# Kernel tuning notes

Measured on AMD Instinct MI355X. Metric: run time of the kernel, lower is better.

The kernel has to match this reference:

```python
import jax, jax.numpy as jnp
import numpy as np

B, S, H = 1, 2048, 4096
NQ, NKV, D = 32, 8, 128
N_REP = NQ // NKV
SCALE = 1.0 / np.sqrt(D)
SOFTCAP = 30.0
EPS = 1e-5


def _rotate_half(x):
    x1, x2 = jnp.split(x, 2, axis=-1)
    return jnp.concatenate([-x2, x1], axis=-1)


def _rms_norm(x, w, eps=EPS):
    xf = x.astype(jnp.float32)
    norm = xf * jax.lax.rsqrt(jnp.mean(xf * xf, axis=-1, keepdims=True) + eps)
    return (w * norm).astype(x.dtype)


def setup_inputs() -> dict:
    key = jax.random.key(0)
    ks = jax.random.split(key, 8)
    hidden_states = jax.random.normal(ks[0], (B, S, H), dtype=jnp.float32)
    # causal additive mask
    causal = jnp.tril(jnp.ones((S, S), dtype=bool))
    attention_mask = jnp.where(causal, 0.0, -1e9)[None, None].astype(jnp.float32)
    # RoPE cache
    inv_freq = 1.0 / (10000.0 ** (np.arange(0, D, 2, dtype=np.float32) / D))
    t = np.arange(S, dtype=np.float32)
    freqs = np.outer(t, inv_freq)                      # (S, D/2)
    emb = np.concatenate([freqs, freqs], axis=-1)      # (S, D)
    cos = jnp.asarray(np.cos(emb))[None, None]         # (1,1,S,D)
    sin = jnp.asarray(np.sin(emb))[None, None]
    # params
    std = 0.02
    wq = jax.random.normal(ks[1], (NQ * D, H), dtype=jnp.float32) * std
    wk = jax.random.normal(ks[2], (NKV * D, H), dtype=jnp.float32) * std
    wv = jax.random.normal(ks[3], (NKV * D, H), dtype=jnp.float32) * std
    wo = jax.random.normal(ks[4], (H, NQ * D), dtype=jnp.float32) * std
    pre_norm_w = jnp.ones((H,), dtype=jnp.float32)
    q_norm_w = jnp.ones((D,), dtype=jnp.float32)
    k_norm_w = jnp.ones((D,), dtype=jnp.float32)
    return {
        "hidden_states": hidden_states, "attention_mask": attention_mask,
        "cos": cos, "sin": sin, "pre_norm_w": pre_norm_w,
        "wq": wq, "wk": wk, "wv": wv, "wo": wo,
        "q_norm_w": q_norm_w, "k_norm_w": k_norm_w,
    }


def reference(hidden_states, attention_mask, cos, sin, pre_norm_w,
              wq, wk, wv, wo, q_norm_w, k_norm_w):
    residual = hidden_states
    h = _rms_norm(hidden_states, pre_norm_w)
    bsz, seq_len, _ = h.shape
    # projections -> (b, heads, s, d)
    q = jnp.einsum('bsh,eh->bse', h, wq).reshape(bsz, seq_len, NQ, D).transpose(0, 2, 1, 3)
    k = jnp.einsum('bsh,eh->bse', h, wk).reshape(bsz, seq_len, NKV, D).transpose(0, 2, 1, 3)
    v = jnp.einsum('bsh,eh->bse', h, wv).reshape(bsz, seq_len, NKV, D).transpose(0, 2, 1, 3)
    # QK RMSNorm over head_dim
    q = _rms_norm(q, q_norm_w)
    k = _rms_norm(k, k_norm_w)
    # RoPE (full head_dim)
    q = q * cos + _rotate_half(q) * sin
    k = k * cos + _rotate_half(k) * sin
    # GQA: repeat kv heads
    k_exp = jnp.repeat(k, N_REP, axis=1)  # (b, NQ, s, d)
    v_exp = jnp.repeat(v, N_REP, axis=1)
    scores = jnp.einsum('bhqd,bhkd->bhqk', q, k_exp) * SCALE
    scores = SOFTCAP * jnp.tanh(scores / SOFTCAP)
    scores = scores + attention_mask
    probs = jax.nn.softmax(scores.astype(jnp.float32), axis=-1).astype(q.dtype)
    attn = jnp.einsum('bhqk,bhkd->bhqd', probs, v_exp)
    attn = attn.transpose(0, 2, 1, 3).reshape(bsz, seq_len, NQ * D)
    out = jnp.einsum('bse,he->bsh', attn, wo)
    return residual + out
```

## Files before the change

### kernel.cpp

```cpp
#include <hip/hip_runtime.h>
#include <cstdint>

typedef __bf16 bf16;
typedef __bf16 bf16x8 __attribute__((ext_vector_type(8)));
typedef __bf16 bf16x4 __attribute__((ext_vector_type(4)));
typedef float  f32x4  __attribute__((ext_vector_type(4)));

#define SEQ  2048
#define HID  4096
#define DH   128
#define NQH  32
#define NKVH 8
#define RSCALE 0.08838834764831845f
#define SOFTCAP 30.0f
#define L2E 1.4426950408889634f

__device__ __forceinline__ void gl2lds16(const void* g, void* l) {
  __builtin_amdgcn_global_load_lds(
      (const __attribute__((address_space(1))) unsigned int*)g,
      (__attribute__((address_space(3))) unsigned int*)l, 16, 0, 0);
}

__global__ void cvt_kernel(const float* __restrict__ in, bf16* __restrict__ out, int n4) {
  const int stride = gridDim.x * blockDim.x;
  for (int i = blockIdx.x * blockDim.x + threadIdx.x; i < n4; i += stride) {
    const float4 v = ((const float4*)in)[i];
    bf16x4 o = { (bf16)v.x, (bf16)v.y, (bf16)v.z, (bf16)v.w };
    *(bf16x4*)(out + (size_t)i * 4) = o;
  }
}

__global__ void rmsnorm_kernel(const float* __restrict__ x, const float* __restrict__ w,
                               bf16* __restrict__ out) {
  const int s = blockIdx.x;
  const float* xr = x + (size_t)s * HID;
  float4 v[4];
  float ss = 0.f;
#pragma unroll
  for (int j = 0; j < 4; ++j) {
    v[j] = ((const float4*)xr)[threadIdx.x + j * 256];
    ss += v[j].x * v[j].x + v[j].y * v[j].y + v[j].z * v[j].z + v[j].w * v[j].w;
  }
#pragma unroll
  for (int m = 1; m < 64; m <<= 1) ss += __shfl_xor(ss, m);
  __shared__ float red[4];
  if ((threadIdx.x & 63) == 0) red[threadIdx.x >> 6] = ss;
  __syncthreads();
  const float rn = rsqrtf((red[0] + red[1] + red[2] + red[3]) * (1.f / HID) + 1e-5f);
  bf16* orow = out + (size_t)s * HID;
#pragma unroll
  for (int j = 0; j < 4; ++j) {
    const int idx = (threadIdx.x + j * 256) * 4;
    const float4 wv = ((const float4*)w)[threadIdx.x + j * 256];
    bf16x4 o = { (bf16)(v[j].x * rn * wv.x), (bf16)(v[j].y * rn * wv.y),
                 (bf16)(v[j].z * rn * wv.z), (bf16)(v[j].w * rn * wv.w) };
    *(bf16x4*)(orow + idx) = o;
  }
}

template<bool FINAL>
__global__ __launch_bounds__(256, 3)
void gemm_bt(const bf16* __restrict__ A, const bf16* __restrict__ B,
             bf16* __restrict__ Cb, float* __restrict__ Cf,
             const float* __restrict__ resid, int M, int N, int K)
{
  __shared__ bf16 As[128 * 64];
  __shared__ bf16 Bs[128 * 64];
  const int tid  = threadIdx.x;
  const int lane = tid & 63;
  const int wave = tid >> 6;
  const int wm = wave >> 1, wn = wave & 1;

  const int gx = gridDim.x;
  const int nwg = gx * gridDim.y;
  int lin = blockIdx.x + gx * blockIdx.y;
  lin = (lin & 7) * (nwg >> 3) + (lin >> 3);
  const int m0 = (lin / gx) * 128, n0 = (lin % gx) * 128;

  f32x4 acc[4][4] = {};

  for (int kt = 0; kt < K; kt += 64) {
#pragma unroll
    for (int i = 0; i < 4; ++i) {
      const int c = wave * 4 + i;
      const int row = c * 8 + (lane >> 3);
      const int col8 = (lane & 7) ^ (row & 7);
      gl2lds16(A + (size_t)(m0 + row) * K + kt + col8 * 8, As + c * 512);
      gl2lds16(B + (size_t)(n0 + row) * K + kt + col8 * 8, Bs + c * 512);
    }
    __syncthreads();
#pragma unroll
    for (int ks = 0; ks < 2; ++ks) {
      bf16x8 af[4], bfv[4];
#pragma unroll
      for (int mi = 0; mi < 4; ++mi) {
        const int row = wm * 64 + mi * 16 + (lane & 15);
        const int slot = (ks * 4 + (lane >> 4)) ^ (row & 7);
        af[mi] = *(const bf16x8*)(As + row * 64 + slot * 8);
      }
#pragma unroll
      for (int ni = 0; ni < 4; ++ni) {
        const int row = wn * 64 + ni * 16 + (lane & 15);
        const int slot = (ks * 4 + (lane >> 4)) ^ (row & 7);
        bfv[ni] = *(const bf16x8*)(Bs + row * 64 + slot * 8);
      }
#pragma unroll
      for (int mi = 0; mi < 4; ++mi)
#pragma unroll
        for (int ni = 0; ni < 4; ++ni)
          acc[mi][ni] = __builtin_amdgcn_mfma_f32_16x16x32_bf16(af[mi], bfv[ni], acc[mi][ni], 0, 0, 0);
    }
    __syncthreads();
  }

#pragma unroll
  for (int mi = 0; mi < 4; ++mi) {
#pragma unroll
    for (int i = 0; i < 4; ++i) {
      const int m = m0 + wm * 64 + mi * 16 + (lane >> 4) * 4 + i;
#pragma unroll
      for (int ni = 0; ni < 4; ++ni) {
        const int n = n0 + wn * 64 + ni * 16 + (lane & 15);
        const float v = acc[mi][ni][i];
        if constexpr (FINAL) {
          Cf[(size_t)m * N + n] = v + resid[(size_t)m * N + n];
        } else {
          Cb[(size_t)m * N + n] = (bf16)v;
        }
      }
    }
  }
}

__global__ void qkrope_kernel(const bf16* __restrict__ qpj, const bf16* __restrict__ kpj,
                              const float* __restrict__ qw, const float* __restrict__ kw,
                              const float* __restrict__ cs, const float* __restrict__ sn,
                              bf16* __restrict__ qr, bf16* __restrict__ kr)
{
  const int w = blockIdx.x * 4 + (threadIdx.x >> 6);
  const int lane = threadIdx.x & 63;
  const int s = w / (NQH + NKVH);
  const int hh = w % (NQH + NKVH);
  const bf16* src; bf16* dst; const float* nw;
  if (hh < NQH) {
    src = qpj + (size_t)s * (NQH * DH) + hh * DH;
    dst = qr + ((size_t)hh * SEQ + s) * DH;
    nw = qw;
  } else {
    const int h2 = hh - NQH;
    src = kpj + (size_t)s * 2048 + h2 * DH;
    dst = kr + ((size_t)h2 * SEQ + s) * DH;
    nw = kw;
  }
  const float x0 = (float)src[lane], x1 = (float)src[lane + 64];
  float ss = x0 * x0 + x1 * x1;
#pragma unroll
  for (int m = 1; m < 64; m <<= 1) ss += __shfl_xor(ss, m);
  const float rn = rsqrtf(ss * (1.f / DH) + 1e-5f);
  const float n0 = x0 * rn * nw[lane], n1 = x1 * rn * nw[lane + 64];
  const float c0 = cs[s * DH + lane],      s0 = sn[s * DH + lane];
  const float c1 = cs[s * DH + lane + 64], s1 = sn[s * DH + lane + 64];
  dst[lane]      = (bf16)(n0 * c0 - n1 * s0);
  dst[lane + 64] = (bf16)(n1 * c1 + n0 * s1);
}

__global__ void vtrans_kernel(const bf16* __restrict__ vsrc, bf16* __restrict__ vt)
{
  __shared__ bf16 tbuf[64][33];
  const int s0 = blockIdx.x * 64;
  const int d0 = blockIdx.y * 32;
  const int h  = blockIdx.z;
  const int tid = threadIdx.x;
  {
    const int col = tid & 31, r0 = tid >> 5;
    for (int r = r0; r < 64; r += 8)
      tbuf[r][col] = vsrc[(size_t)(s0 + r) * 2048 + 1024 + h * DH + d0 + col];
  }
  __syncthreads();
  {
    const int sc = tid & 63, dr0 = tid >> 6;
    for (int d = dr0; d < 32; d += 4)
      vt[((size_t)h * DH + d0 + d) * SEQ + s0 + sc] = tbuf[sc][d];
  }
}

__global__ __launch_bounds__(256, 2)
void attn_kernel(const bf16* __restrict__ Q, const bf16* __restrict__ Kr,
                 const bf16* __restrict__ Vt, bf16* __restrict__ Oa)
{
  __shared__ bf16 Ks[2][64 * 128];
  __shared__ bf16 Vs[2][128 * 64];
  __shared__ bf16 Ps[4][32 * 64];

  const int tid = threadIdx.x, lane = tid & 63, wave = tid >> 6;

  const int lin  = blockIdx.x + 16 * blockIdx.y;
  const int slot = lin >> 8, idx = lin & 255;
  const int bx   = slot ? (15 - (idx & 15)) : (idx & 15);
  const int head = (slot << 4) | (idx >> 4);
  const int kvh  = head >> 2;
  const int q0   = bx * 128;
  const int wq0  = q0 + wave * 32;

  const bf16* Qh = Q  + (size_t)head * SEQ * DH;
  const bf16* Kh = Kr + (size_t)kvh * SEQ * DH;
  const bf16* Vh = Vt + (size_t)kvh * DH * SEQ;

  bf16x8 qf[2][4];
#pragma unroll
  for (int mt = 0; mt < 2; ++mt)
#pragma unroll
    for (int kc = 0; kc < 4; ++kc) {
      const int r = wq0 + mt * 16 + (lane & 15);
      qf[mt][kc] = *(const bf16x8*)(Qh + (size_t)r * DH + kc * 32 + (lane >> 4) * 8);
    }

  float lsum[2][4] = {};
  f32x4 o_acc[2][8] = {};

  const int ntiles = q0 / 64 + 2;

  auto stage = [&](int t, int b) {
    const int kv0 = t * 64;
    bf16* Kd = &Ks[b][0];
    bf16* Vd = &Vs[b][0];
#pragma unroll
    for (int i2 = 0; i2 < 4; ++i2) {
      const int c = wave * 4 + i2;
      {
        const int row = c * 4 + (lane >> 4);
        const int col8 = (lane & 15) ^ (row & 15);
        gl2lds16(Kh + (size_t)(kv0 + row) * DH + col8 * 8, Kd + c * 512);
      }
      {
        const int row = c * 8 + (lane >> 3);
        const int col8 = (lane & 7) ^ (row & 7);
        gl2lds16(Vh + (size_t)row * SEQ + kv0 + col8 * 8, Vd + c * 512);
      }
    }
  };

  stage(0, 0);
  __syncthreads();

  const float ZS = RSCALE / SOFTCAP;
  const float A1 = RSCALE * L2E;
  const float B3 = -(ZS * ZS) * (1.f / 3.f);
  const float B5 = (2.f / 15.f) * (ZS * ZS) * (ZS * ZS);
  const float C  = SOFTCAP * L2E;

  for (int t = 0; t < ntiles; ++t) {
    const int cur = t & 1;
    if (t + 1 < ntiles) stage(t + 1, cur ^ 1);
    const int kv0 = t * 64;
    const bf16* Kb = &Ks[cur][0];
    const bf16* Vb = &Vs[cur][0];

    if (kv0 <= wq0 + 31) {
      f32x4 sc[2][4] = {};
      __builtin_amdgcn_s_setprio(1);
#pragma unroll
      for (int ks = 0; ks < 4; ++ks) {
        bf16x8 kf[4];
#pragma unroll
        for (int nt = 0; nt < 4; ++nt) {
          const int row = nt * 16 + (lane & 15);
          const int sl = (ks * 4 + (lane >> 4)) ^ (row & 15);
          kf[nt] = *(const bf16x8*)(Kb + row * 128 + sl * 8);
        }
#pragma unroll
        for (int mt = 0; mt < 2; ++mt)
#pragma unroll
          for (int nt = 0; nt < 4; ++nt)
            sc[mt][nt] = __builtin_amdgcn_mfma_f32_16x16x32_bf16(qf[mt][ks], kf[nt], sc[mt][nt], 0, 0, 0);
      }
      __builtin_amdgcn_s_setprio(0);

      if (kv0 + 63 <= wq0) {
#pragma unroll
        for (int mt = 0; mt < 2; ++mt)
#pragma unroll
          for (int i = 0; i < 4; ++i)
#pragma unroll
            for (int nt = 0; nt < 4; ++nt) {
              const float s = sc[mt][nt][i];
              const float w = s * s;
              const float poly = fmaf(fmaf(B5, w, B3), w, 1.f);
              const float p = __builtin_amdgcn_exp2f(fmaf(s * poly, A1, -C));
              sc[mt][nt][i] = p;
              lsum[mt][i] += p;
            }
      } else {
#pragma unroll
        for (int mt = 0; mt < 2; ++mt)
#pragma unroll
          for (int i = 0; i < 4; ++i) {
            const int qrow = wq0 + mt * 16 + (lane >> 4) * 4 + i;
#pragma unroll
            for (int nt = 0; nt < 4; ++nt) {
              const int col = kv0 + nt * 16 + (lane & 15);
              const float s = sc[mt][nt][i];
              const float w = s * s;
              const float poly = fmaf(fmaf(B5, w, B3), w, 1.f);
              float p = __builtin_amdgcn_exp2f(fmaf(s * poly, A1, -C));
              if (col > qrow) p = 0.f;
              sc[mt][nt][i] = p;
              lsum[mt][i] += p;
            }
          }
      }

#pragma unroll
      for (int mt = 0; mt < 2; ++mt)
#pragma unroll
        for (int nt = 0; nt < 4; ++nt)
#pragma unroll
          for (int i = 0; i < 4; ++i) {
            const int r = mt * 16 + (lane >> 4) * 4 + i;
            const int colb = nt * 16 + (lane & 15);
            const int sl = (colb >> 3) ^ (r & 7);
            Ps[wave][r * 64 + sl * 8 + (colb & 7)] = (bf16)sc[mt][nt][i];
          }
      asm volatile("s_waitcnt lgkmcnt(0)" ::: "memory");
      __builtin_amdgcn_sched_barrier(0);

      __builtin_amdgcn_s_setprio(1);
#pragma unroll
      for (int ks2 = 0; ks2 < 2; ++ks2) {
        bf16x8 pf[2];
#pragma unroll
        for (int mt = 0; mt < 2; ++mt) {
          const int r = mt * 16 + (lane & 15);
          const int sl = (ks2 * 4 + (lane >> 4)) ^ (r & 7);
          pf[mt] = *(const bf16x8*)(&Ps[wave][r * 64 + sl * 8]);
        }
#pragma unroll
        for (int nt = 0; nt < 8; ++nt) {
          const int row = nt * 16 + (lane & 15);
          const int sl = (ks2 * 4 + (lane >> 4)) ^ (row & 7);
          const bf16x8 vf = *(const bf16x8*)(Vb + row * 64 + sl * 8);
          o_acc[0][nt] = __builtin_amdgcn_mfma_f32_16x16x32_bf16(pf[0], vf, o_acc[0][nt], 0, 0, 0);
          o_acc[1][nt] = __builtin_amdgcn_mfma_f32_16x16x32_bf16(pf[1], vf, o_acc[1][nt], 0, 0, 0);
        }
      }
      __builtin_amdgcn_s_setprio(0);
    }
    __syncthreads();
  }

#pragma unroll
  for (int mt = 0; mt < 2; ++mt)
#pragma unroll
    for (int i = 0; i < 4; ++i) {
      float l = lsum[mt][i];
#pragma unroll
      for (int m = 1; m < 16; m <<= 1) l += __shfl_xor(l, m);
      const int qrow = wq0 + mt * 16 + (lane >> 4) * 4 + i;
      const float inv_l = 1.f / l;
#pragma unroll
      for (int nt = 0; nt < 8; ++nt) {
        const int d = nt * 16 + (lane & 15);
        Oa[(size_t)qrow * HID + head * DH + d] = (bf16)(o_acc[mt][nt][i] * inv_l);
      }
    }
}

extern "C" void kernel_launch(void* const* d_in, const int* in_sizes, int n_in,
                              void* d_out, int out_size, void* d_ws, size_t ws_size,
                              hipStream_t stream)
{
  const float* hidden = (const float*)d_in[0];
  const float* cosb   = (const float*)d_in[2];
  const float* sinb   = (const float*)d_in[3];
  const float* prew   = (const float*)d_in[4];
  const float* wq     = (const float*)d_in[5];
  const float* wk     = (const float*)d_in[6];
  const float* wv     = (const float*)d_in[7];
  const float* wo     = (const float*)d_in[8];
  const float* qnw    = (const float*)d_in[9];
  const float* knw    = (const float*)d_in[10];
  float* outp = (float*)d_out;
  char* ws = (char*)d_ws;

  bf16* wqb  = (bf16*)(ws + 0);
  bf16* wkvb = (bf16*)(ws + 33554432);
  bf16* kvpj = (bf16*)(ws + 50331648);
  bf16* hb   = (bf16*)(ws + 58720256);
  bf16* qpj  = (bf16*)(ws + 75497472);
  bf16* kr   = (bf16*)(ws + 92274688);
  bf16* vt   = (bf16*)(ws + 96468992);

  cvt_kernel<<<2048, 256, 0, stream>>>(wq, wqb, (NQH * DH) * HID / 4);
  cvt_kernel<<<1024, 256, 0, stream>>>(wk, wkvb, (NKVH * DH) * HID / 4);
  cvt_kernel<<<1024, 256, 0, stream>>>(wv, wkvb + (size_t)(NKVH * DH) * HID, (NKVH * DH) * HID / 4);
  rmsnorm_kernel<<<SEQ, 256, 0, stream>>>(hidden, prew, hb);

  gemm_bt<false><<<dim3(32, 16), 256, 0, stream>>>(hb, wqb,  qpj,  nullptr, nullptr, SEQ, 4096, 4096);
  gemm_bt<false><<<dim3(16, 16), 256, 0, stream>>>(hb, wkvb, kvpj, nullptr, nullptr, SEQ, 2048, 4096);

  qkrope_kernel<<<SEQ * (NQH + NKVH) / 4, 256, 0, stream>>>(qpj, kvpj, qnw, knw, cosb, sinb, hb, kr);
  vtrans_kernel<<<dim3(32, 4, 8), 256, 0, stream>>>(kvpj, vt);
  cvt_kernel<<<2048, 256, 0, stream>>>(wo, wqb, (NQH * DH) * HID / 4);

  attn_kernel<<<dim3(16, 32), 256, 0, stream>>>(hb, kr, vt, qpj);

  gemm_bt<true><<<dim3(32, 16), 256, 0, stream>>>(qpj, wqb, nullptr, outp, hidden, SEQ, 4096, 4096);
}
```

Before: 376.2 us.

## Fuse QKV projections into one GEMM and shrink attention KV tile to 32

Q, K and V weights are converted into one contiguous buffer so a single GEMM with N=6144 produces all projections. This removes one launch and fills the GPU better than two separate GEMMs. The attention kernel's KV tile drops from 64 to 32 rows, which shrinks shared memory and raises launch bounds to 4 blocks per SU, with swizzles adjusted to match. The cost is more loop iterations and more barriers per tile, and the downstream kernels now index a 6144-wide row layout.

```diff
diff --git a/kernel.cpp b/kernel.cpp
--- a/kernel.cpp
+++ b/kernel.cpp
@@ -11,6 +11,7 @@
 #define DH   128
 #define NQH  32
 #define NKVH 8
+#define NTOT 6144
 #define RSCALE 0.08838834764831845f
 #define SOFTCAP 30.0f
 #define L2E 1.4426950408889634f
@@ -132,7 +133,7 @@
   }
 }
 
-__global__ void qkrope_kernel(const bf16* __restrict__ qpj, const bf16* __restrict__ kpj,
+__global__ void qkrope_kernel(const bf16* __restrict__ qkv,
                               const float* __restrict__ qw, const float* __restrict__ kw,
                               const float* __restrict__ cs, const float* __restrict__ sn,
                               bf16* __restrict__ qr, bf16* __restrict__ kr)
@@ -143,12 +144,12 @@
   const int hh = w % (NQH + NKVH);
   const bf16* src; bf16* dst; const float* nw;
   if (hh < NQH) {
-    src = qpj + (size_t)s * (NQH * DH) + hh * DH;
+    src = qkv + (size_t)s * NTOT + hh * DH;
     dst = qr + ((size_t)hh * SEQ + s) * DH;
     nw = qw;
   } else {
     const int h2 = hh - NQH;
-    src = kpj + (size_t)s * 2048 + h2 * DH;
+    src = qkv + (size_t)s * NTOT + 4096 + h2 * DH;
     dst = kr + ((size_t)h2 * SEQ + s) * DH;
     nw = kw;
   }
@@ -164,7 +165,7 @@
   dst[lane + 64] = (bf16)(n1 * c1 + n0 * s1);
 }
 
-__global__ void vtrans_kernel(const bf16* __restrict__ vsrc, bf16* __restrict__ vt)
+__global__ void vtrans_kernel(const bf16* __restrict__ qkv, bf16* __restrict__ vt)
 {
   __shared__ bf16 tbuf[64][33];
   const int s0 = blockIdx.x * 64;
@@ -174,7 +175,7 @@
   {
     const int col = tid & 31, r0 = tid >> 5;
     for (int r = r0; r < 64; r += 8)
-      tbuf[r][col] = vsrc[(size_t)(s0 + r) * 2048 + 1024 + h * DH + d0 + col];
+      tbuf[r][col] = qkv[(size_t)(s0 + r) * NTOT + 5120 + h * DH + d0 + col];
   }
   __syncthreads();
   {
@@ -184,15 +185,16 @@
   }
 }
 
-__global__ __launch_bounds__(256, 2)
+__global__ __launch_bounds__(256, 4)
 void attn_kernel(const bf16* __restrict__ Q, const bf16* __restrict__ Kr,
                  const bf16* __restrict__ Vt, bf16* __restrict__ Oa)
 {
-  __shared__ bf16 Ks[2][64 * 128];
-  __shared__ bf16 Vs[2][128 * 64];
-  __shared__ bf16 Ps[4][32 * 64];
+  __shared__ bf16 Ks[2][32 * 128];
+  __shared__ bf16 Vs[2][128 * 32];
+  __shared__ bf16 Ps[4][32 * 32];
 
   const int tid = threadIdx.x, lane = tid & 63, wave = tid >> 6;
+  const int rl = lane & 15, hi = lane >> 4;
 
   const int lin  = blockIdx.x + 16 * blockIdx.y;
   const int slot = lin >> 8, idx = lin & 255;
@@ -211,31 +213,31 @@
   for (int mt = 0; mt < 2; ++mt)
 #pragma unroll
     for (int kc = 0; kc < 4; ++kc) {
-      const int r = wq0 + mt * 16 + (lane & 15);
-      qf[mt][kc] = *(const bf16x8*)(Qh + (size_t)r * DH + kc * 32 + (lane >> 4) * 8);
+      const int r = wq0 + mt * 16 + rl;
+      qf[mt][kc] = *(const bf16x8*)(Qh + (size_t)r * DH + kc * 32 + hi * 8);
     }
 
   float lsum[2][4] = {};
   f32x4 o_acc[2][8] = {};
 
-  const int ntiles = q0 / 64 + 2;
+  const int ntiles = q0 / 32 + 4;
 
   auto stage = [&](int t, int b) {
-    const int kv0 = t * 64;
+    const int kv0 = t * 32;
     bf16* Kd = &Ks[b][0];
     bf16* Vd = &Vs[b][0];
 #pragma unroll
-    for (int i2 = 0; i2 < 4; ++i2) {
-      const int c = wave * 4 + i2;
+    for (int i2 = 0; i2 < 2; ++i2) {
+      const int c = wave * 2 + i2;
       {
         const int row = c * 4 + (lane >> 4);
         const int col8 = (lane & 15) ^ (row & 15);
         gl2lds16(Kh + (size_t)(kv0 + row) * DH + col8 * 8, Kd + c * 512);
       }
       {
-        const int row = c * 8 + (lane >> 3);
-        const int col8 = (lane & 7) ^ (row & 7);
-        gl2lds16(Vh + (size_t)row * SEQ + kv0 + col8 * 8, Vd + c * 512);
+        const int row = c * 16 + (lane >> 2);
+        const int s = (lane & 3) ^ ((row >> 1) & 3);
+        gl2lds16(Vh + (size_t)row * SEQ + kv0 + s * 8, Vd + c * 512);
       }
     }
   };
@@ -252,37 +254,37 @@
   for (int t = 0; t < ntiles; ++t) {
     const int cur = t & 1;
     if (t + 1 < ntiles) stage(t + 1, cur ^ 1);
-    const int kv0 = t * 64;
+    const int kv0 = t * 32;
     const bf16* Kb = &Ks[cur][0];
     const bf16* Vb = &Vs[cur][0];
 
     if (kv0 <= wq0 + 31) {
-      f32x4 sc[2][4] = {};
+      f32x4 sc[2][2] = {};
       __builtin_amdgcn_s_setprio(1);
 #pragma unroll
       for (int ks = 0; ks < 4; ++ks) {
-        bf16x8 kf[4];
-#pragma unroll
-        for (int nt = 0; nt < 4; ++nt) {
-          const int row = nt * 16 + (lane & 15);
-          const int sl = (ks * 4 + (lane >> 4)) ^ (row & 15);
+        bf16x8 kf[2];
+#pragma unroll
+        for (int nt = 0; nt < 2; ++nt) {
+          const int row = nt * 16 + rl;
+          const int sl = (ks * 4 + hi) ^ (row & 15);
           kf[nt] = *(const bf16x8*)(Kb + row * 128 + sl * 8);
         }
 #pragma unroll
         for (int mt = 0; mt < 2; ++mt)
 #pragma unroll
-          for (int nt = 0; nt < 4; ++nt)
+          for (int nt = 0; nt < 2; ++nt)
             sc[mt][nt] = __builtin_amdgcn_mfma_f32_16x16x32_bf16(qf[mt][ks], kf[nt], sc[mt][nt], 0, 0, 0);
       }
       __builtin_amdgcn_s_setprio(0);
 
-      if (kv0 + 63 <= wq0) {
+      if (kv0 < wq0) {
 #pragma unroll
         for (int mt = 0; mt < 2; ++mt)
 #pragma unroll
           for (int i = 0; i < 4; ++i)
 #pragma unroll
-            for (int nt = 0; nt < 4; ++nt) {
+            for (int nt = 0; nt < 2; ++nt) {
               const float s = sc[mt][nt][i];
               const float w = s * s;
               const float poly = fmaf(fmaf(B5, w, B3), w, 1.f);
@@ -295,10 +297,10 @@
         for (int mt = 0; mt < 2; ++mt)
 #pragma unroll
           for (int i = 0; i < 4; ++i) {
-            const int qrow = wq0 + mt * 16 + (lane >> 4) * 4 + i;
-#pragma unroll
-            for (int nt = 0; nt < 4; ++nt) {
-              const int col = kv0 + nt * 16 + (lane & 15);
+            const int qrow = wq0 + mt * 16 + hi * 4 + i;
+#pragma unroll
+            for (int nt = 0; nt < 2; ++nt) {
+              const int col = kv0 + nt * 16 + rl;
               const float s = sc[mt][nt][i];
               const float w = s * s;
               const float poly = fmaf(fmaf(B5, w, B3), w, 1.f);
@@ -313,35 +315,32 @@
 #pragma unroll
       for (int mt = 0; mt < 2; ++mt)
 #pragma unroll
-        for (int nt = 0; nt < 4; ++nt)
+        for (int nt = 0; nt < 2; ++nt)
 #pragma unroll
           for (int i = 0; i < 4; ++i) {
-            const int r = mt * 16 + (lane >> 4) * 4 + i;
-            const int colb = nt * 16 + (lane & 15);
-            const int sl = (colb >> 3) ^ (r & 7);
-            Ps[wave][r * 64 + sl * 8 + (colb & 7)] = (bf16)sc[mt][nt][i];
+            const int r = mt * 16 + hi * 4 + i;
+            const int colb = nt * 16 + rl;
+            const int sl = (colb >> 3) ^ ((r >> 1) & 3);
+            Ps[wave][r * 32 + sl * 8 + (colb & 7)] = (bf16)sc[mt][nt][i];
           }
       asm volatile("s_waitcnt lgkmcnt(0)" ::: "memory");
       __builtin_amdgcn_sched_barrier(0);
 
       __builtin_amdgcn_s_setprio(1);
-#pragma unroll
-      for (int ks2 = 0; ks2 < 2; ++ks2) {
-        bf16x8 pf[2];
-#pragma unroll
-        for (int mt = 0; mt < 2; ++mt) {
-          const int r = mt * 16 + (lane & 15);
-          const int sl = (ks2 * 4 + (lane >> 4)) ^ (r & 7);
-          pf[mt] = *(const bf16x8*)(&Ps[wave][r * 64 + sl * 8]);
-        }
-#pragma unroll
-        for (int nt = 0; nt < 8; ++nt) {
-          const int row = nt * 16 + (lane & 15);
-          const int sl = (ks2 * 4 + (lane >> 4)) ^ (row & 7);
-          const bf16x8 vf = *(const bf16x8*)(Vb + row * 64 + sl * 8);
-          o_acc[0][nt] = __builtin_amdgcn_mfma_f32_16x16x32_bf16(pf[0], vf, o_acc[0][nt], 0, 0, 0);
-          o_acc[1][nt] = __builtin_amdgcn_mfma_f32_16x16x32_bf16(pf[1], vf, o_acc[1][nt], 0, 0, 0);
-        }
+      bf16x8 pf[2];
+#pragma unroll
+      for (int mt = 0; mt < 2; ++mt) {
+        const int r = mt * 16 + rl;
+        const int sl = hi ^ ((r >> 1) & 3);
+        pf[mt] = *(const bf16x8*)(&Ps[wave][r * 32 + sl * 8]);
+      }
+#pragma unroll
+      for (int nt = 0; nt < 8; ++nt) {
+        const int row = nt * 16 + rl;
+        const int sl = hi ^ ((row >> 1) & 3);
+        const bf16x8 vf = *(const bf16x8*)(Vb + row * 32 + sl * 8);
+        o_acc[0][nt] = __builtin_amdgcn_mfma_f32_16x16x32_bf16(pf[0], vf, o_acc[0][nt], 0, 0, 0);
+        o_acc[1][nt] = __builtin_amdgcn_mfma_f32_16x16x32_bf16(pf[1], vf, o_acc[1][nt], 0, 0, 0);
       }
       __builtin_amdgcn_s_setprio(0);
     }
@@ -355,11 +354,11 @@
       float l = lsum[mt][i];
 #pragma unroll
       for (int m = 1; m < 16; m <<= 1) l += __shfl_xor(l, m);
-      const int qrow = wq0 + mt * 16 + (lane >> 4) * 4 + i;
+      const int qrow = wq0 + mt * 16 + hi * 4 + i;
       const float inv_l = 1.f / l;
 #pragma unroll
       for (int nt = 0; nt < 8; ++nt) {
-        const int d = nt * 16 + (lane & 15);
+        const int d = nt * 16 + rl;
         Oa[(size_t)qrow * HID + head * DH + d] = (bf16)(o_acc[mt][nt][i] * inv_l);
       }
     }
@@ -382,27 +381,28 @@
   float* outp = (float*)d_out;
   char* ws = (char*)d_ws;
 
-  bf16* wqb  = (bf16*)(ws + 0);
-  bf16* wkvb = (bf16*)(ws + 33554432);
-  bf16* kvpj = (bf16*)(ws + 50331648);
-  bf16* hb   = (bf16*)(ws + 58720256);
-  bf16* qpj  = (bf16*)(ws + 75497472);
+  bf16* wqkv = (bf16*)(ws + 0);
+  bf16* hb   = (bf16*)(ws + 50331648);
+  bf16* qkvp = (bf16*)(ws + 67108864);
   bf16* kr   = (bf16*)(ws + 92274688);
   bf16* vt   = (bf16*)(ws + 96468992);
-
-  cvt_kernel<<<2048, 256, 0, stream>>>(wq, wqb, (NQH * DH) * HID / 4);
-  cvt_kernel<<<1024, 256, 0, stream>>>(wk, wkvb, (NKVH * DH) * HID / 4);
-  cvt_kernel<<<1024, 256, 0, stream>>>(wv, wkvb + (size_t)(NKVH * DH) * HID, (NKVH * DH) * HID / 4);
+  bf16* wob  = wqkv;
+
+  cvt_kernel<<<2048, 256, 0, stream>>>(wq, wqkv, 4096 * HID / 4);
+  cvt_kernel<<<1024, 256, 0, stream>>>(wk, wqkv + (size_t)4096 * HID, 1024 * HID / 4);
+  cvt_kernel<<<1024, 256, 0, stream>>>(wv, wqkv + (size_t)5120 * HID, 1024 * HID / 4);
   rmsnorm_kernel<<<SEQ, 256, 0, stream>>>(hidden, prew, hb);
 
-  gemm_bt<false><<<dim3(32, 16), 256, 0, stream>>>(hb, wqb,  qpj,  nullptr, nullptr, SEQ, 4096, 4096);
-  gemm_bt<false><<<dim3(16, 16), 256, 0, stream>>>(hb, wkvb, kvpj, nullptr, nullptr, SEQ, 2048, 4096);
-
-  qkrope_kernel<<<SEQ * (NQH + NKVH) / 4, 256, 0, stream>>>(qpj, kvpj, qnw, knw, cosb, sinb, hb, kr);
-  vtrans_kernel<<<dim3(32, 4, 8), 256, 0, stream>>>(kvpj, vt);
-  cvt_kernel<<<2048, 256, 0, stream>>>(wo, wqb, (NQH * DH) * HID / 4);
-
-  attn_kernel<<<dim3(16, 32), 256, 0, stream>>>(hb, kr, vt, qpj);
-
-  gemm_bt<true><<<dim3(32, 16), 256, 0, stream>>>(qpj, wqb, nullptr, outp, hidden, SEQ, 4096, 4096);
-}
+  gemm_bt<false><<<dim3(NTOT / 128, SEQ / 128), 256, 0, stream>>>(
+      hb, wqkv, qkvp, nullptr, nullptr, SEQ, NTOT, HID);
+
+  cvt_kernel<<<2048, 256, 0, stream>>>(wo, wob, HID * HID / 4);
+
+  qkrope_kernel<<<SEQ * (NQH + NKVH) / 4, 256, 0, stream>>>(qkvp, qnw, knw, cosb, sinb, hb, kr);
+  vtrans_kernel<<<dim3(32, 4, 8), 256, 0, stream>>>(qkvp, vt);
+
+  attn_kernel<<<dim3(16, 32), 256, 0, stream>>>(hb, kr, vt, qkvp);
+
+  gemm_bt<true><<<dim3(HID / 128, SEQ / 128), 256, 0, stream>>>(
+      qkvp, wob, nullptr, outp, hidden, SEQ, HID, HID);
+}
```

Measured after the change: 671.7 us. 78.5% more time.
